# Performance work log

Measured on AMD Instinct MI355X. Metric: run time of the kernel, lower is better.

## Reference

```python
import jax, jax.numpy as jnp
import numpy as np

# Model dims (see init_kwargs)
E = 512        # embedding_dim
H = 1536       # hidden_dim
SIZE = 4       # state_space.size (state types per layer)
S = 32         # choices per state type (uniform state size)
L = 12         # num_layers of child network
T = SIZE * L   # total controller steps = 48
V = SIZE * S   # num_embeddings = 128


def setup_inputs() -> dict:
    key = jax.random.key(0)
    ks = jax.random.split(key, 12)
    sc = 0.05
    f32 = jnp.float32
    return {
        "input_id": 0,
        "emb":   (jax.random.normal(ks[0], (V, E)) * sc).astype(f32),
        "W_ih1": (jax.random.normal(ks[1], (4 * H, E)) * sc).astype(f32),
        "W_hh1": (jax.random.normal(ks[2], (4 * H, H)) * sc).astype(f32),
        "b_ih1": (jax.random.normal(ks[3], (4 * H,)) * sc).astype(f32),
        "b_hh1": (jax.random.normal(ks[4], (4 * H,)) * sc).astype(f32),
        "W_ih2": (jax.random.normal(ks[5], (4 * H, H)) * sc).astype(f32),
        "W_hh2": (jax.random.normal(ks[6], (4 * H, H)) * sc).astype(f32),
        "b_ih2": (jax.random.normal(ks[7], (4 * H,)) * sc).astype(f32),
        "b_hh2": (jax.random.normal(ks[8], (4 * H,)) * sc).astype(f32),
        "W_out": (jax.random.normal(ks[9], (T, S, H)) * sc).astype(f32),
        "b_out": (jax.random.normal(ks[10], (T, S)) * sc).astype(f32),
    }


def _lstm_cell(x, h, c, Wih, Whh, bih, bhh):
    # torch.nn.LSTMCell: gates ordered (i, f, g, o)
    g = x @ Wih.T + bih + h @ Whh.T + bhh
    gi, gf, gg, go = jnp.split(g, 4)
    c_new = jax.nn.sigmoid(gf) * c + jax.nn.sigmoid(gi) * jnp.tanh(gg)
    h_new = jax.nn.sigmoid(go) * jnp.tanh(c_new)
    return h_new, c_new


def reference(input_id, emb, W_ih1, W_hh1, b_ih1, b_hh1,
              W_ih2, W_hh2, b_ih2, b_hh2, W_out, b_out):
    x0 = emb[input_id]                      # [E]
    z = jnp.zeros((H,), emb.dtype)

    def step(carry, inp):
        i, Wo, bo = inp                     # Wo: [S,H], bo: [S]
        x, h1, c1, h2, c2 = carry
        h1, c1 = _lstm_cell(x, h1, c1, W_ih1, W_hh1, b_ih1, b_hh1)
        h2, c2 = _lstm_cell(h1, h2, c2, W_ih2, W_hh2, b_ih2, b_hh2)
        logp = jax.nn.log_softmax(Wo @ h2 + bo)   # [S]
        pred = jnp.argmax(logp)
        emb_id = (i % SIZE) * S + pred            # state-space embedding id
        x_next = emb[emb_id]
        return (x_next, h1, c1, h2, c2), logp

    _, scores = jax.lax.scan(step, (x0, z, z, z, z),
                             (jnp.arange(T), W_out, b_out))
    return scores  # [T, S] log-probabilities
```

## Files before the change

### kernel.cpp

```cpp
#include <hip/hip_runtime.h>
#include <math.h>

#define H 1536
#define E 512
#define T 48
#define S 32
#define V 128
#define NB 256
#define BT 512
#define NWV 8
#define JPB 6
#define ROWS 24
#define RPW 3
#define CHK 24
#define WHH2_B   (64 * 145 * 16)
#define HBUF_B   (64 * 7 * 16)
#define DYN_LDS  (WHH2_B + 2 * HBUF_B)

__device__ __forceinline__ float sigf(float x) { return 1.0f / (1.0f + expf(-x)); }
__device__ __forceinline__ float wred(float acc) {
#pragma unroll
    for (int off = 32; off; off >>= 1) acc += __shfl_down(acc, off);
    return acc;
}

#define GLD(p)    __hip_atomic_load((p), __ATOMIC_RELAXED, __HIP_MEMORY_SCOPE_AGENT)
#define GST(p, v) __hip_atomic_store((p), (v), __ATOMIC_RELAXED, __HIP_MEMORY_SCOPE_AGENT)

__device__ __forceinline__ void gbar(unsigned* flags, unsigned* rel, unsigned& gen) {
    __syncthreads();
    gen++;
    if (blockIdx.x == 0) {
        if (threadIdx.x < 64) {
            const int i0 = threadIdx.x * 4;
            for (;;) {
                unsigned a0 = (i0 == 0) ? gen : GLD(&flags[(i0 + 0) * 16]);
                unsigned a1 = GLD(&flags[(i0 + 1) * 16]);
                unsigned a2 = GLD(&flags[(i0 + 2) * 16]);
                unsigned a3 = GLD(&flags[(i0 + 3) * 16]);
                bool ok = (a0 >= gen) && (a1 >= gen) && (a2 >= gen) && (a3 >= gen);
                if (__all(ok)) break;
                __builtin_amdgcn_s_sleep(1);
            }
#pragma unroll
            for (int k = 0; k < 4; ++k) GST(&rel[(i0 + k) * 16], gen);
        }
    } else {
        if (threadIdx.x == 0) {
            GST(&flags[blockIdx.x * 16], gen);
            while (GLD(&rel[blockIdx.x * 16]) < gen) __builtin_amdgcn_s_sleep(1);
        }
    }
    __syncthreads();
}

__global__ void init_kernel(unsigned* u) {
    for (int i = threadIdx.x; i < 8192; i += 256) u[i] = 0u;
}

__global__ __launch_bounds__(BT, 2) void nas_persist(
    const int* __restrict__ input_id, const float* __restrict__ emb,
    const float* __restrict__ Wih1, const float* __restrict__ Whh1,
    const float* __restrict__ bih1, const float* __restrict__ bhh1,
    const float* __restrict__ Wih2, const float* __restrict__ Whh2,
    const float* __restrict__ bih2, const float* __restrict__ bhh2,
    const float* __restrict__ Wout, const float* __restrict__ bout,
    float* __restrict__ out, float* __restrict__ ws)
{
    const int b = blockIdx.x, tid = threadIdx.x;
    const int wave = tid >> 6, lane = tid & 63;

    unsigned* rel   = (unsigned*)ws;
    unsigned* flags = (unsigned*)ws + 4096;
    float* h1g  = ws + 8192;
    float* h2g  = ws + 8192 + H;
    float* xw1g = ws + 16384 + (size_t)b * (V * ROWS);

    extern __shared__ char dyn_lds[];
    float4* whh2s = (float4*)dyn_lds;
    float*  h1s   = (float*)(dyn_lds + WHH2_B);
    float*  h2s   = (float*)(dyn_lds + WHH2_B + HBUF_B);

    __shared__ float gacc1[ROWS], g2f[ROWS], bsum2[ROWS], zlog[S], xr[ROWS];
    __shared__ float c1s[JPB], c2s[JPB];
    __shared__ int   xid_s;

    unsigned gen = 0;

    if (tid < JPB) { c1s[tid] = 0.f; c2s[tid] = 0.f; }
    if (tid < ROWS) {
        int r = (tid / JPB) * H + b * JPB + (tid % JPB);
        bsum2[tid] = bih2[r] + bhh2[r];
    }
    if (tid == 0) xid_s = *input_id;

    {
        const int k0 = wave * RPW;
        float4 wiA[RPW], wiB[RPW];
        float  bs[RPW];
#pragma unroll
        for (int i = 0; i < RPW; ++i) {
            int k = k0 + i;
            int r = (k / JPB) * H + b * JPB + (k % JPB);
            const float4* w = (const float4*)(Wih1 + (size_t)r * E);
            wiA[i] = w[lane]; wiB[i] = w[lane + 64];
            bs[i]  = bih1[r] + bhh1[r];
        }
        float4* stage = (float4*)dyn_lds;
        for (int ch = 0; ch < 8; ++ch) {
            const float4* src = (const float4*)(emb + (size_t)ch * 16 * E);
            for (int m = tid; m < 2048; m += BT) stage[m] = src[m];
            __syncthreads();
            for (int vv = 0; vv < 16; ++vv) {
                float4 ea = stage[vv * 128 + lane];
                float4 eb = stage[vv * 128 + 64 + lane];
#pragma unroll
                for (int i = 0; i < RPW; ++i) {
                    float a = wiA[i].x * ea.x + wiA[i].y * ea.y + wiA[i].z * ea.z + wiA[i].w * ea.w
                            + wiB[i].x * eb.x + wiB[i].y * eb.y + wiB[i].z * eb.z + wiB[i].w * eb.w;
                    a = wred(a);
                    if (lane == 0) xw1g[(ch * 16 + vv) * ROWS + (k0 + i)] = a + bs[i];
                }
            }
            __syncthreads();
        }
    }

    for (int k = 0; k < ROWS; ++k) {
        int r = (k / JPB) * H + b * JPB + (k % JPB);
        const float4* src = (const float4*)(Whh2 + (size_t)r * H);
        if (tid < 384) {
            int l = tid / 6, j = tid % 6;
            whh2s[l * 145 + k * 6 + j] = src[tid];
        }
    }
    __syncthreads();

    float w1[RPW][CHK], w2[RPW][CHK];
#pragma unroll
    for (int i = 0; i < RPW; ++i) {
        int k = wave * RPW + i;
        int r = (k / JPB) * H + b * JPB + (k % JPB);
        const float4* p1 = (const float4*)(Whh1 + (size_t)r * H) + lane * 6;
        const float4* p2 = (const float4*)(Wih2 + (size_t)r * H) + lane * 6;
#pragma unroll
        for (int j = 0; j < 6; ++j) {
            float4 v1 = p1[j], v2 = p2[j];
            w1[i][4 * j + 0] = v1.x; w1[i][4 * j + 1] = v1.y;
            w1[i][4 * j + 2] = v1.z; w1[i][4 * j + 3] = v1.w;
            w2[i][4 * j + 0] = v2.x; w2[i][4 * j + 1] = v2.y;
            w2[i][4 * j + 2] = v2.z; w2[i][4 * j + 3] = v2.w;
        }
    }

    float h2c[CHK];
#pragma unroll
    for (int k = 0; k < CHK; ++k) h2c[k] = 0.f;

    __syncthreads();
    if (tid < ROWS) xr[tid] = xw1g[xid_s * ROWS + tid];
    __syncthreads();
    if (tid < JPB) {
        float gi = xr[tid], gg = xr[2 * JPB + tid], go = xr[3 * JPB + tid];
        float cn = sigf(gi) * tanhf(gg);
        c1s[tid] = cn;
        GST(h1g + b * JPB + tid, sigf(go) * tanhf(cn));
    }
    gbar(flags, rel, gen);

    for (int t = 0; t < T; ++t) {
        for (int i = tid; i < H; i += BT)
            h1s[(i / CHK) * 28 + (i % CHK)] = GLD(h1g + i);
        __syncthreads();

        float h1c[CHK];
        {
            const float4* hp = (const float4*)h1s + lane * 7;
#pragma unroll
            for (int j = 0; j < 6; ++j) {
                float4 v = hp[j];
                h1c[4 * j + 0] = v.x; h1c[4 * j + 1] = v.y;
                h1c[4 * j + 2] = v.z; h1c[4 * j + 3] = v.w;
            }
        }
        float a1[RPW], a2[RPW];
#pragma unroll
        for (int i = 0; i < RPW; ++i) { a1[i] = 0.f; a2[i] = 0.f; }
#pragma unroll
        for (int k = 0; k < CHK; ++k) {
            float h = h1c[k];
#pragma unroll
            for (int i = 0; i < RPW; ++i) {
                a1[i] += w1[i][k] * h;
                a2[i] += w2[i][k] * h;
            }
        }
#pragma unroll
        for (int i = 0; i < RPW; ++i) {
            int k = wave * RPW + i;
            const float4* wp = whh2s + lane * 145 + k * 6;
            float ah = 0.f;
#pragma unroll
            for (int j = 0; j < 6; ++j) {
                float4 v = wp[j];
                ah += v.x * h2c[4 * j + 0] + v.y * h2c[4 * j + 1]
                    + v.z * h2c[4 * j + 2] + v.w * h2c[4 * j + 3];
            }
            float s1 = wred(a1[i]);
            float s2 = wred(a2[i] + ah);
            if (lane == 0) {
                gacc1[k] = s1;
                g2f[k]   = s2 + bsum2[k];
            }
        }
        __syncthreads();
        if (tid < JPB) {
            float gi = g2f[tid],           gf = g2f[JPB + tid];
            float gg = g2f[2 * JPB + tid], go = g2f[3 * JPB + tid];
            float cn = sigf(gf) * c2s[tid] + sigf(gi) * tanhf(gg);
            c2s[tid] = cn;
            GST(h2g + b * JPB + tid, sigf(go) * tanhf(cn));
        }
        gbar(flags, rel, gen);

        for (int i = tid; i < H; i += BT)
            h2s[(i / CHK) * 28 + (i % CHK)] = GLD(h2g + i);
        __syncthreads();
        {
            const float4* hp = (const float4*)h2s + lane * 7;
#pragma unroll
            for (int j = 0; j < 6; ++j) {
                float4 v = hp[j];
                h2c[4 * j + 0] = v.x; h2c[4 * j + 1] = v.y;
                h2c[4 * j + 2] = v.z; h2c[4 * j + 3] = v.w;
            }
        }
#pragma unroll
        for (int q = 0; q < 4; ++q) {
            int s = wave * 4 + q;
            const float4* wo = (const float4*)(Wout + ((size_t)t * S + s) * H) + lane * 6;
            float acc = 0.f;
#pragma unroll
            for (int j = 0; j < 6; ++j) {
                float4 v = wo[j];
                acc += v.x * h2c[4 * j + 0] + v.y * h2c[4 * j + 1]
                     + v.z * h2c[4 * j + 2] + v.w * h2c[4 * j + 3];
            }
            acc = wred(acc);
            if (lane == 0) zlog[s] = acc + bout[t * S + s];
        }
        __syncthreads();
        if (wave == 0) {
            float z = (lane < S) ? zlog[lane] : -1e30f;
            float v = z; int idx = (lane < S) ? lane : 9999;
#pragma unroll
            for (int off = 32; off; off >>= 1) {
                float ov = __shfl_xor(v, off); int oi = __shfl_xor(idx, off);
                if (ov > v || (ov == v && oi < idx)) { v = ov; idx = oi; }
            }
            float e = (lane < S) ? expf(z - v) : 0.f;
#pragma unroll
            for (int off = 32; off; off >>= 1) e += __shfl_xor(e, off);
            if (lane == 0) xid_s = (t & 3) * S + idx;
            if (b == 0 && lane < S) out[(size_t)t * S + lane] = z - v - logf(e);
        }
        __syncthreads();
        if (tid < ROWS) xr[tid] = xw1g[xid_s * ROWS + tid];
        __syncthreads();
        if (tid < JPB) {
            float gi = gacc1[tid]           + xr[tid];
            float gf = gacc1[JPB + tid]     + xr[JPB + tid];
            float gg = gacc1[2 * JPB + tid] + xr[2 * JPB + tid];
            float go = gacc1[3 * JPB + tid] + xr[3 * JPB + tid];
            float cn = sigf(gf) * c1s[tid] + sigf(gi) * tanhf(gg);
            c1s[tid] = cn;
            GST(h1g + b * JPB + tid, sigf(go) * tanhf(cn));
        }
        gbar(flags, rel, gen);
    }
}

extern "C" void kernel_launch(void* const* d_in, const int* in_sizes, int n_in,
                              void* d_out, int out_size, void* d_ws, size_t ws_size,
                              hipStream_t stream) {
    const int*   input_id = (const int*)d_in[0];
    const float* emb  = (const float*)d_in[1];
    const float* Wih1 = (const float*)d_in[2];
    const float* Whh1 = (const float*)d_in[3];
    const float* bih1 = (const float*)d_in[4];
    const float* bhh1 = (const float*)d_in[5];
    const float* Wih2 = (const float*)d_in[6];
    const float* Whh2 = (const float*)d_in[7];
    const float* bih2 = (const float*)d_in[8];
    const float* bhh2 = (const float*)d_in[9];
    const float* Wout = (const float*)d_in[10];
    const float* bout = (const float*)d_in[11];
    float* out = (float*)d_out;
    float* ws  = (float*)d_ws;

    init_kernel<<<1, 256, 0, stream>>>((unsigned*)ws);

    void* args[] = { (void*)&input_id, (void*)&emb,
                     (void*)&Wih1, (void*)&Whh1, (void*)&bih1, (void*)&bhh1,
                     (void*)&Wih2, (void*)&Whh2, (void*)&bih2, (void*)&bhh2,
                     (void*)&Wout, (void*)&bout, (void*)&out, (void*)&ws };
    hipLaunchCooperativeKernel((void*)nas_persist, dim3(NB), dim3(BT), args,
                               DYN_LDS, stream);
}
```

Measured before the change: 1.221 ms.

## Speculate all 32 layer-1 candidates to cut one grid barrier per step

Before the argmax of step t is known, each block computes layer-1 LSTM outputs for all 32 possible next tokens and writes them to double-buffered global candidate arrays. Each step then needs one grid barrier instead of two. After the barrier, every block evaluates the output logits redundantly, picks the winning candidate and loads its h1. The Whh2·h2 product is also moved to right after h2 is loaded. This adds 32x more layer-1 elementwise work and more global traffic for the candidate arrays, but removes a device-wide synchronisation from the serial critical path.

```diff
diff --git a/kernel.cpp b/kernel.cpp
--- a/kernel.cpp
+++ b/kernel.cpp
@@ -8,14 +8,13 @@
 #define V 128
 #define NB 256
 #define BT 512
-#define NWV 8
 #define JPB 6
 #define ROWS 24
 #define RPW 3
 #define CHK 24
 #define WHH2_B   (64 * 145 * 16)
 #define HBUF_B   (64 * 7 * 16)
-#define DYN_LDS  (WHH2_B + 2 * HBUF_B)
+#define DYN_LDS  (WHH2_B + HBUF_B)
 
 __device__ __forceinline__ float sigf(float x) { return 1.0f / (1.0f + expf(-x)); }
 __device__ __forceinline__ float wred(float acc) {
@@ -72,25 +71,25 @@
 
     unsigned* rel   = (unsigned*)ws;
     unsigned* flags = (unsigned*)ws + 4096;
-    float* h1g  = ws + 8192;
-    float* h2g  = ws + 8192 + H;
-    float* xw1g = ws + 16384 + (size_t)b * (V * ROWS);
+    float* h2gp[2]  = { ws + 8192, ws + 8192 + H };
+    float* candp[2] = { ws + 16384, ws + 16384 + S * H };
+    float* xw1g = ws + 114688 + (size_t)b * (V * ROWS);
 
     extern __shared__ char dyn_lds[];
     float4* whh2s = (float4*)dyn_lds;
-    float*  h1s   = (float*)(dyn_lds + WHH2_B);
-    float*  h2s   = (float*)(dyn_lds + WHH2_B + HBUF_B);
-
-    __shared__ float gacc1[ROWS], g2f[ROWS], bsum2[ROWS], zlog[S], xr[ROWS];
-    __shared__ float c1s[JPB], c2s[JPB];
-    __shared__ int   xid_s;
+    float*  hbuf  = (float*)(dyn_lds + WHH2_B);
+
+    __shared__ float gacc1[ROWS], gaccH[ROWS], g2f[ROWS], bsum2[ROWS], zlog[S];
+    __shared__ float c1s[JPB], c2s[JPB], c1cand[S * JPB];
+    __shared__ int   xid_s, pred_s;
 
     unsigned gen = 0;
 
-    if (tid < JPB) { c1s[tid] = 0.f; c2s[tid] = 0.f; }
+    if (tid < JPB) { c2s[tid] = 0.f; GST(h2gp[0] + b * JPB + tid, 0.f); }
     if (tid < ROWS) {
         int r = (tid / JPB) * H + b * JPB + (tid % JPB);
         bsum2[tid] = bih2[r] + bhh2[r];
+        gaccH[tid] = 0.f;
     }
     if (tid == 0) xid_s = *input_id;
 
@@ -152,30 +151,96 @@
             w2[i][4 * j + 2] = v2.z; w2[i][4 * j + 3] = v2.w;
         }
     }
-
-    float h2c[CHK];
-#pragma unroll
-    for (int k = 0; k < CHK; ++k) h2c[k] = 0.f;
-
     __syncthreads();
-    if (tid < ROWS) xr[tid] = xw1g[xid_s * ROWS + tid];
-    __syncthreads();
+
     if (tid < JPB) {
+        const float* xr = xw1g + (size_t)xid_s * ROWS;
         float gi = xr[tid], gg = xr[2 * JPB + tid], go = xr[3 * JPB + tid];
         float cn = sigf(gi) * tanhf(gg);
         c1s[tid] = cn;
-        GST(h1g + b * JPB + tid, sigf(go) * tanhf(cn));
+        GST(candp[0] + b * JPB + tid, sigf(go) * tanhf(cn));
     }
     gbar(flags, rel, gen);
 
-    for (int t = 0; t < T; ++t) {
-        for (int i = tid; i < H; i += BT)
-            h1s[(i / CHK) * 28 + (i % CHK)] = GLD(h1g + i);
+    for (int k = 0; k <= T; ++k) {
+        {
+            const float* src = h2gp[k & 1];
+            for (int i = tid; i < H; i += BT)
+                hbuf[(i / CHK) * 28 + (i % CHK)] = GLD(src + i);
+        }
         __syncthreads();
-
+        float h2c[CHK];
+        {
+            const float4* hp = (const float4*)hbuf + lane * 7;
+#pragma unroll
+            for (int j = 0; j < 6; ++j) {
+                float4 v = hp[j];
+                h2c[4 * j + 0] = v.x; h2c[4 * j + 1] = v.y;
+                h2c[4 * j + 2] = v.z; h2c[4 * j + 3] = v.w;
+            }
+        }
+        __syncthreads();
+
+        int psel = 0;
+        if (k > 0) {
+#pragma unroll
+            for (int q = 0; q < 4; ++q) {
+                int s = wave * 4 + q;
+                const float4* wo = (const float4*)(Wout + ((size_t)(k - 1) * S + s) * H) + lane * 6;
+                float acc = 0.f;
+#pragma unroll
+                for (int j = 0; j < 6; ++j) {
+                    float4 v = wo[j];
+                    acc += v.x * h2c[4 * j + 0] + v.y * h2c[4 * j + 1]
+                         + v.z * h2c[4 * j + 2] + v.w * h2c[4 * j + 3];
+                }
+                acc = wred(acc);
+                if (lane == 0) zlog[s] = acc + bout[(k - 1) * S + s];
+            }
+#pragma unroll
+            for (int i = 0; i < RPW; ++i) {
+                int kk = wave * RPW + i;
+                const float4* wp = whh2s + lane * 145 + kk * 6;
+                float ah = 0.f;
+#pragma unroll
+                for (int j = 0; j < 6; ++j) {
+                    float4 v = wp[j];
+                    ah += v.x * h2c[4 * j + 0] + v.y * h2c[4 * j + 1]
+                        + v.z * h2c[4 * j + 2] + v.w * h2c[4 * j + 3];
+                }
+                ah = wred(ah);
+                if (lane == 0) gaccH[kk] = ah;
+            }
+            __syncthreads();
+            if (wave == 0) {
+                float z = (lane < S) ? zlog[lane] : -1e30f;
+                float v = z; int idx = (lane < S) ? lane : 9999;
+#pragma unroll
+                for (int off = 32; off; off >>= 1) {
+                    float ov = __shfl_xor(v, off); int oi = __shfl_xor(idx, off);
+                    if (ov > v || (ov == v && oi < idx)) { v = ov; idx = oi; }
+                }
+                float e = (lane < S) ? expf(z - v) : 0.f;
+#pragma unroll
+                for (int off = 32; off; off >>= 1) e += __shfl_xor(e, off);
+                if (lane == 0) pred_s = idx;
+                if (b == 0 && lane < S) out[(size_t)(k - 1) * S + lane] = z - v - logf(e);
+            }
+            __syncthreads();
+            if (k == T) return;
+            psel = pred_s;
+            if (tid < JPB) c1s[tid] = c1cand[psel * JPB + tid];
+        }
+
+        {
+            const float* src = candp[k & 1] + (size_t)psel * H;
+            for (int i = tid; i < H; i += BT)
+                hbuf[(i / CHK) * 28 + (i % CHK)] = GLD(src + i);
+        }
+        __syncthreads();
         float h1c[CHK];
         {
-            const float4* hp = (const float4*)h1s + lane * 7;
+            const float4* hp = (const float4*)hbuf + lane * 7;
 #pragma unroll
             for (int j = 0; j < 6; ++j) {
                 float4 v = hp[j];
@@ -187,94 +252,44 @@
 #pragma unroll
         for (int i = 0; i < RPW; ++i) { a1[i] = 0.f; a2[i] = 0.f; }
 #pragma unroll
-        for (int k = 0; k < CHK; ++k) {
-            float h = h1c[k];
+        for (int kk = 0; kk < CHK; ++kk) {
+            float h = h1c[kk];
 #pragma unroll
             for (int i = 0; i < RPW; ++i) {
-                a1[i] += w1[i][k] * h;
-                a2[i] += w2[i][k] * h;
+                a1[i] += w1[i][kk] * h;
+                a2[i] += w2[i][kk] * h;
             }
         }
 #pragma unroll
         for (int i = 0; i < RPW; ++i) {
-            int k = wave * RPW + i;
-            const float4* wp = whh2s + lane * 145 + k * 6;
-            float ah = 0.f;
-#pragma unroll
-            for (int j = 0; j < 6; ++j) {
-                float4 v = wp[j];
-                ah += v.x * h2c[4 * j + 0] + v.y * h2c[4 * j + 1]
-                    + v.z * h2c[4 * j + 2] + v.w * h2c[4 * j + 3];
-            }
+            int kk = wave * RPW + i;
             float s1 = wred(a1[i]);
-            float s2 = wred(a2[i] + ah);
+            float s2 = wred(a2[i]);
             if (lane == 0) {
-                gacc1[k] = s1;
-                g2f[k]   = s2 + bsum2[k];
+                gacc1[kk] = s1;
+                g2f[kk]   = s2 + gaccH[kk] + bsum2[kk];
             }
         }
         __syncthreads();
+
         if (tid < JPB) {
             float gi = g2f[tid],           gf = g2f[JPB + tid];
             float gg = g2f[2 * JPB + tid], go = g2f[3 * JPB + tid];
             float cn = sigf(gf) * c2s[tid] + sigf(gi) * tanhf(gg);
             c2s[tid] = cn;
-            GST(h2g + b * JPB + tid, sigf(go) * tanhf(cn));
-        }
-        gbar(flags, rel, gen);
-
-        for (int i = tid; i < H; i += BT)
-            h2s[(i / CHK) * 28 + (i % CHK)] = GLD(h2g + i);
-        __syncthreads();
-        {
-            const float4* hp = (const float4*)h2s + lane * 7;
-#pragma unroll
-            for (int j = 0; j < 6; ++j) {
-                float4 v = hp[j];
-                h2c[4 * j + 0] = v.x; h2c[4 * j + 1] = v.y;
-                h2c[4 * j + 2] = v.z; h2c[4 * j + 3] = v.w;
-            }
-        }
-#pragma unroll
-        for (int q = 0; q < 4; ++q) {
-            int s = wave * 4 + q;
-            const float4* wo = (const float4*)(Wout + ((size_t)t * S + s) * H) + lane * 6;
-            float acc = 0.f;
-#pragma unroll
-            for (int j = 0; j < 6; ++j) {
-                float4 v = wo[j];
-                acc += v.x * h2c[4 * j + 0] + v.y * h2c[4 * j + 1]
-                     + v.z * h2c[4 * j + 2] + v.w * h2c[4 * j + 3];
-            }
-            acc = wred(acc);
-            if (lane == 0) zlog[s] = acc + bout[t * S + s];
-        }
-        __syncthreads();
-        if (wave == 0) {
-            float z = (lane < S) ? zlog[lane] : -1e30f;
-            float v = z; int idx = (lane < S) ? lane : 9999;
-#pragma unroll
-            for (int off = 32; off; off >>= 1) {
-                float ov = __shfl_xor(v, off); int oi = __shfl_xor(idx, off);
-                if (ov > v || (ov == v && oi < idx)) { v = ov; idx = oi; }
-            }
-            float e = (lane < S) ? expf(z - v) : 0.f;
-#pragma unroll
-            for (int off = 32; off; off >>= 1) e += __shfl_xor(e, off);
-            if (lane == 0) xid_s = (t & 3) * S + idx;
-            if (b == 0 && lane < S) out[(size_t)t * S + lane] = z - v - logf(e);
-        }
-        __syncthreads();
-        if (tid < ROWS) xr[tid] = xw1g[xid_s * ROWS + tid];
-        __syncthreads();
-        if (tid < JPB) {
-            float gi = gacc1[tid]           + xr[tid];
-            float gf = gacc1[JPB + tid]     + xr[JPB + tid];
-            float gg = gacc1[2 * JPB + tid] + xr[2 * JPB + tid];
-            float go = gacc1[3 * JPB + tid] + xr[3 * JPB + tid];
-            float cn = sigf(gf) * c1s[tid] + sigf(gi) * tanhf(gg);
-            c1s[tid] = cn;
-            GST(h1g + b * JPB + tid, sigf(go) * tanhf(cn));
+            GST(h2gp[(k + 1) & 1] + b * JPB + tid, sigf(go) * tanhf(cn));
+        }
+        if (tid < S * JPB) {
+            int p = tid / JPB, j = tid % JPB;
+            const float* xr = xw1g + (size_t)((k & 3) * S + p) * ROWS;
+            float gi = gacc1[j]           + xr[j];
+            float gf = gacc1[JPB + j]     + xr[JPB + j];
+            float gg = gacc1[2 * JPB + j] + xr[2 * JPB + j];
+            float go = gacc1[3 * JPB + j] + xr[3 * JPB + j];
+            float cn = sigf(gf) * c1s[j] + sigf(gi) * tanhf(gg);
+            c1cand[tid] = cn;
+            GST(candp[(k + 1) & 1] + (size_t)p * H + b * JPB + j,
+                sigf(go) * tanhf(cn));
         }
         gbar(flags, rel, gen);
     }
```

Result: faster. 1.176 ms (-3.7%).
